# Performance work log

Hardware: AMD Instinct MI355X
Metric: run time of the kernel (lower is better)

The kernel has to match this reference:

```python
import jax, jax.numpy as jnp
import numpy as np

N = 100000   # nodes
E = 800000   # edges
IN = 256     # input feature dim
H = 4        # heads per layer
D = 32       # per-head hidden dim (num_hidden)
SLOPE = 0.2  # leaky_relu negative slope


def setup_inputs() -> dict:
    key = jax.random.key(0)
    ks = jax.random.split(key, 8)
    s = 0.1  # weight scale for numerical stability
    x = jax.random.normal(ks[0], (N, IN), jnp.float32)
    edge_index = jax.random.randint(ks[1], (2, E), 0, N, dtype=jnp.int32)
    W0 = jax.random.normal(ks[2], (IN, H * D), jnp.float32) * s
    al0 = jax.random.normal(ks[3], (H, D), jnp.float32) * s
    ar0 = jax.random.normal(ks[4], (H, D), jnp.float32) * s
    W1 = jax.random.normal(ks[5], (H * D, H * D), jnp.float32) * s
    al1 = jax.random.normal(ks[6], (H, D), jnp.float32) * s
    ar1 = jax.random.normal(ks[7], (H, D), jnp.float32) * s
    return {"x": x, "edge_index": edge_index, "W0": W0, "al0": al0,
            "ar0": ar0, "W1": W1, "al1": al1, "ar1": ar1}


def _gat_layer(h, W, al, ar, src, dst, residual):
    """One GATConv: project, edge attention, dst-wise softmax, scatter-agg."""
    n = h.shape[0]
    feat = (h @ W).reshape(n, H, D)              # [N,H,D]
    el = jnp.einsum('nhd,hd->nh', feat, al)      # [N,H]
    er = jnp.einsum('nhd,hd->nh', feat, ar)      # [N,H]
    e = jax.nn.leaky_relu(el[src] + er[dst], SLOPE)   # raw scores [E,H]
    # edge softmax grouped by destination node (numerically stable)
    emax = jax.ops.segment_max(e, dst, num_segments=n)   # [N,H]
    eexp = jnp.exp(e - emax[dst])                          # [E,H]
    denom = jax.ops.segment_sum(eexp, dst, num_segments=n)  # [N,H]
    a = eexp / denom[dst]                                  # attention [E,H]
    msg = feat[src] * a[:, :, None]                        # [E,H,D]
    rst = jax.ops.segment_sum(msg, dst, num_segments=n)    # [N,H,D]
    if residual:
        rst = rst + h.reshape(n, H, D)  # identity residual (dims match)
    rst = jax.nn.elu(rst)               # activation
    return rst, a, e


def reference(x, edge_index, W0, al0, ar0, W1, al1, ar1):
    src, dst = edge_index[0], edge_index[1]
    # layer 0: no residual
    h1, a0, e0 = _gat_layer(x, W0, al0, ar0, src, dst, residual=False)
    atten0 = e0.mean(axis=-1)  # e_gat.flatten(1).mean(-1) -> [E]
    # layer 1: residual
    h2, a1, e1 = _gat_layer(h1.reshape(N, H * D), W1, al1, ar1, src, dst,
                            residual=True)
    atten1 = e1.mean(axis=-1)
    temp = h2.reshape(N, H * D)          # flattened node embeddings
    heads = tuple(h2[:, i] for i in range(H))  # per-head [N,D]
    return (temp,) + heads + (e1, atten0, atten1)
```

## Files before the change

kernel.cpp:

```cpp
#include <hip/hip_runtime.h>
#include <hip/hip_bf16.h>


typedef _Float16 f16;
typedef _Float16 f16x2 __attribute__((ext_vector_type(2)));
typedef _Float16 f16x8 __attribute__((ext_vector_type(8)));
typedef float f32x2 __attribute__((ext_vector_type(2)));
typedef float f32x4 __attribute__((ext_vector_type(4)));

__device__ __forceinline__ void gload16(const void* g, void* l) {
    __builtin_amdgcn_global_load_lds(
        (const __attribute__((address_space(1))) unsigned int*)g,
        (__attribute__((address_space(3))) unsigned int*)l, 16, 0, 0);
}

__global__ void prep(const float* __restrict__ W0, const float* __restrict__ W1,
                     f16* __restrict__ Wth0, f16* __restrict__ Wtl0,
                     f16* __restrict__ Wth1, f16* __restrict__ Wtl1,
                     const int* __restrict__ dsts, int* __restrict__ deg, int E) {
    int i = blockIdx.x * blockDim.x + threadIdx.x;
    if (i < 256 * 128) {
        int k = i >> 7, c = i & 127;
        float v = W0[i];
        f16 h = (f16)v;
        Wth0[(size_t)c * 256 + k] = h;
        Wtl0[(size_t)c * 256 + k] = (f16)(v - (float)h);
    } else if (i < 256 * 128 + 128 * 128) {
        int j = i - 256 * 128;
        int k = j >> 7, c = j & 127;
        float v = W1[j];
        f16 h = (f16)v;
        Wth1[(size_t)c * 128 + k] = h;
        Wtl1[(size_t)c * 128 + k] = (f16)(v - (float)h);
    } else {
        int e = i - (256 * 128 + 128 * 128);
        if (e < E) atomicAdd(&deg[dsts[e]], 1);
    }
}

template <int AFP16>
__global__ __launch_bounds__(256, 2) void gemm_mfma(
        const void* __restrict__ Xv, const f16* __restrict__ Wth,
        const f16* __restrict__ Wtl, f16* __restrict__ Y16,
        const float* __restrict__ al, const float* __restrict__ ar,
        float* __restrict__ el_out, float* __restrict__ er_out,
        int nrows, int K) {
    __shared__ float As32[AFP16 ? 1 : 128 * 32];
    __shared__ f16   As16[AFP16 ? 128 * 32 : 1];
    __shared__ f16   Bh[128 * 32];
    __shared__ f16   Bl[128 * 32];
    const int t    = threadIdx.x;
    const int wave = t >> 6;
    const int lane = t & 63;
    const int lr   = lane & 15;
    const int kg   = lane >> 4;
    const int row0 = blockIdx.x * 128;

    f32x4 acc[2][8];
    #pragma unroll
    for (int i = 0; i < 2; ++i)
        #pragma unroll
        for (int j = 0; j < 8; ++j) acc[i][j] = (f32x4){0.f, 0.f, 0.f, 0.f};

    for (int k0 = 0; k0 < K; k0 += 32) {
        if constexpr (!AFP16) {
            #pragma unroll
            for (int j = 0; j < 4; ++j) {
                int G = t + 256 * j;
                int row = G >> 3, slot = G & 7;
                int g = slot ^ (row & 7);
                int grow = row0 + row; if (grow >= nrows) grow = nrows - 1;
                gload16((const float*)Xv + (size_t)grow * K + k0 + g * 4,
                        &As32[G * 4]);
            }
        } else {
            #pragma unroll
            for (int j = 0; j < 2; ++j) {
                int G = t + 256 * j;
                int row = G >> 2, g4 = G & 3;
                int grow = row0 + row; if (grow >= nrows) grow = nrows - 1;
                gload16((const f16*)Xv + (size_t)grow * K + k0 + g4 * 8,
                        &As16[G * 8]);
            }
        }
        #pragma unroll
        for (int j = 0; j < 2; ++j) {
            int G = t + 256 * j;
            int r = G >> 2, g4 = G & 3;
            int p = ((r & 15) << 3) | (r >> 4);
            gload16(Wth + (size_t)p * K + k0 + g4 * 8, &Bh[G * 8]);
            gload16(Wtl + (size_t)p * K + k0 + g4 * 8, &Bl[G * 8]);
        }
        __syncthreads();

        const int ar0_ = wave * 32 + lr;
        f16x8 ah0, ah1, alo0, alo1;
        if constexpr (!AFP16) {
            int s0 = (2 * kg) ^ (lr & 7);
            int s1 = (2 * kg + 1) ^ (lr & 7);
            f32x4 u0 = *(const f32x4*)&As32[ar0_ * 32 + s0 * 4];
            f32x4 u1 = *(const f32x4*)&As32[ar0_ * 32 + s1 * 4];
            f32x4 v0 = *(const f32x4*)&As32[(ar0_ + 16) * 32 + s0 * 4];
            f32x4 v1 = *(const f32x4*)&As32[(ar0_ + 16) * 32 + s1 * 4];
            float a8[8] = {u0[0], u0[1], u0[2], u0[3], u1[0], u1[1], u1[2], u1[3]};
            float b8[8] = {v0[0], v0[1], v0[2], v0[3], v1[0], v1[1], v1[2], v1[3]};
            #pragma unroll
            for (int i = 0; i < 8; ++i) {
                f16 h0 = (f16)a8[i]; ah0[i] = h0; alo0[i] = (f16)(a8[i] - (float)h0);
                f16 h1 = (f16)b8[i]; ah1[i] = h1; alo1[i] = (f16)(b8[i] - (float)h1);
            }
        } else {
            ah0 = *(const f16x8*)&As16[ar0_ * 32 + kg * 8];
            ah1 = *(const f16x8*)&As16[(ar0_ + 16) * 32 + kg * 8];
        }
        f16x8 bh[8];
        #pragma unroll
        for (int cb = 0; cb < 8; ++cb)
            bh[cb] = *(const f16x8*)&Bh[(cb * 16 + lr) * 32 + kg * 8];

        #pragma unroll
        for (int cb = 0; cb < 8; ++cb) {
            acc[0][cb] = __builtin_amdgcn_mfma_f32_16x16x32_f16(ah0, bh[cb], acc[0][cb], 0, 0, 0);
            acc[1][cb] = __builtin_amdgcn_mfma_f32_16x16x32_f16(ah1, bh[cb], acc[1][cb], 0, 0, 0);
        }
        if constexpr (!AFP16) {
            #pragma unroll
            for (int cb = 0; cb < 8; ++cb) {
                acc[0][cb] = __builtin_amdgcn_mfma_f32_16x16x32_f16(alo0, bh[cb], acc[0][cb], 0, 0, 0);
                acc[1][cb] = __builtin_amdgcn_mfma_f32_16x16x32_f16(alo1, bh[cb], acc[1][cb], 0, 0, 0);
            }
        }
        #pragma unroll
        for (int cb = 0; cb < 8; ++cb) {
            f16x8 bl = *(const f16x8*)&Bl[(cb * 16 + lr) * 32 + kg * 8];
            acc[0][cb] = __builtin_amdgcn_mfma_f32_16x16x32_f16(ah0, bl, acc[0][cb], 0, 0, 0);
            acc[1][cb] = __builtin_amdgcn_mfma_f32_16x16x32_f16(ah1, bl, acc[1][cb], 0, 0, 0);
        }
        __syncthreads();
    }

    const int hh = lr >> 2;
    const int co = (lr & 3) * 8;
    float alv[8], arv[8];
    #pragma unroll
    for (int j = 0; j < 8; ++j) {
        alv[j] = al[hh * 32 + co + j];
        arv[j] = ar[hh * 32 + co + j];
    }
    #pragma unroll
    for (int rb = 0; rb < 2; ++rb) {
        int rbase = row0 + wave * 32 + rb * 16 + kg * 4;
        #pragma unroll
        for (int r = 0; r < 4; ++r) {
            int grow = rbase + r;
            f16x8 hv;
            float sl_ = 0.0f, sr_ = 0.0f;
            #pragma unroll
            for (int cb = 0; cb < 8; ++cb) {
                float v = acc[rb][cb][r];
                hv[cb] = (f16)v;
                sl_ += v * alv[cb];
                sr_ += v * arv[cb];
            }
            sl_ += __shfl_xor(sl_, 1); sl_ += __shfl_xor(sl_, 2);
            sr_ += __shfl_xor(sr_, 1); sr_ += __shfl_xor(sr_, 2);
            if (grow < nrows) {
                *(f16x8*)(Y16 + (size_t)grow * 128 + lr * 8) = hv;
                if ((lane & 3) == 0) {
                    el_out[4 * (size_t)grow + hh] = sl_;
                    er_out[4 * (size_t)grow + hh] = sr_;
                }
            }
        }
    }
}

__global__ __launch_bounds__(256) void scan_block(const int* __restrict__ deg,
                                                  int* __restrict__ excl,
                                                  int* __restrict__ bsums, int n) {
    __shared__ int wsums[4];
    int t = threadIdx.x;
    int base = blockIdx.x * 1024;
    int idx = base + t * 4;
    int v[4];
    #pragma unroll
    for (int i = 0; i < 4; ++i) v[i] = (idx + i < n) ? deg[idx + i] : 0;
    int tsum = v[0] + v[1] + v[2] + v[3];
    int lane = t & 63, wid = t >> 6;
    int incl = tsum;
    #pragma unroll
    for (int off = 1; off < 64; off <<= 1) {
        int u = __shfl_up(incl, off, 64);
        if (lane >= off) incl += u;
    }
    if (lane == 63) wsums[wid] = incl;
    __syncthreads();
    if (t == 0) {
        int s = 0;
        #pragma unroll
        for (int w = 0; w < 4; ++w) { int x = wsums[w]; wsums[w] = s; s += x; }
    }
    __syncthreads();
    int ex = incl - tsum + wsums[wid];
    int run = ex;
    #pragma unroll
    for (int i = 0; i < 4; ++i) { if (idx + i < n) excl[idx + i] = run; run += v[i]; }
    if (t == 255) bsums[blockIdx.x] = ex + tsum;
}

__global__ __launch_bounds__(256) void scan_fin(int* __restrict__ row_off,
                                                const int* __restrict__ bsums,
                                                int* __restrict__ cursor,
                                                int n, int nb) {
    __shared__ int spfx;
    int b = blockIdx.x;
    int t = threadIdx.x;
    if (t < 64) {
        int v = 0;
        if (t < b && t < nb) v = bsums[t];
        int t2 = t + 64;
        if (t2 < b && t2 < nb) v += bsums[t2];
        #pragma unroll
        for (int off = 32; off; off >>= 1) v += __shfl_xor(v, off, 64);
        if (t == 0) spfx = v;
    }
    __syncthreads();
    int pfx = spfx;
    int base = b * 1024 + t * 4;
    #pragma unroll
    for (int i2 = 0; i2 < 4; ++i2) {
        int i = base + i2;
        if (i < n) {
            int v = row_off[i] + pfx;
            row_off[i] = v;
            cursor[i]  = v;
        }
    }
}

__global__ void fill_csr_edge0(const int* __restrict__ srcs, const int* __restrict__ dsts,
                               int* __restrict__ cursor, int* __restrict__ csr_src,
                               const float* __restrict__ el, const float* __restrict__ er,
                               float* __restrict__ atten0, int E) {
    int e = blockIdx.x * blockDim.x + threadIdx.x;
    if (e >= E) return;
    int s = srcs[e], d = dsts[e];
    int p = atomicAdd(&cursor[d], 1);
    csr_src[p] = s;
    float4 elv = *(const float4*)(el + 4 * (size_t)s);
    float4 erv = *(const float4*)(er + 4 * (size_t)d);
    float v0 = elv.x + erv.x, v1 = elv.y + erv.y;
    float v2 = elv.z + erv.z, v3 = elv.w + erv.w;
    v0 = v0 > 0.0f ? v0 : 0.2f * v0;
    v1 = v1 > 0.0f ? v1 : 0.2f * v1;
    v2 = v2 > 0.0f ? v2 : 0.2f * v2;
    v3 = v3 > 0.0f ? v3 : 0.2f * v3;
    __builtin_nontemporal_store((v0 + v1 + v2 + v3) * 0.25f, atten0 + e);
}

__global__ void edge1_kernel(const int* __restrict__ srcs, const int* __restrict__ dsts,
                             const float* __restrict__ el, const float* __restrict__ er,
                             float* __restrict__ e1_out, float* __restrict__ atten1,
                             int E) {
    int e = blockIdx.x * blockDim.x + threadIdx.x;
    if (e >= E) return;
    int s = srcs[e], d = dsts[e];
    float4 elv = *(const float4*)(el + 4 * (size_t)s);
    float4 erv = *(const float4*)(er + 4 * (size_t)d);
    float v0 = elv.x + erv.x, v1 = elv.y + erv.y;
    float v2 = elv.z + erv.z, v3 = elv.w + erv.w;
    v0 = v0 > 0.0f ? v0 : 0.2f * v0;
    v1 = v1 > 0.0f ? v1 : 0.2f * v1;
    v2 = v2 > 0.0f ? v2 : 0.2f * v2;
    v3 = v3 > 0.0f ? v3 : 0.2f * v3;
    __builtin_nontemporal_store((f32x4){v0, v1, v2, v3},
                                (f32x4*)(e1_out + 4 * (size_t)e));
    __builtin_nontemporal_store((v0 + v1 + v2 + v3) * 0.25f, atten1 + e);
}

template <int LAYER>
__global__ __launch_bounds__(256) void aggregate(const int* __restrict__ row_off,
                                                 const int* __restrict__ deg,
                                                 const int* __restrict__ csr_src,
                                                 const float* __restrict__ el,
                                                 const float* __restrict__ er,
                                                 const f16* __restrict__ feat16,
                                                 const f16* __restrict__ resid16,
                                                 f16* __restrict__ out16,
                                                 float* __restrict__ out32,
                                                 float* __restrict__ heads,
                                                 int N) {
    int wave = (blockIdx.x * 256 + threadIdx.x) >> 6;
    if (wave >= N) return;
    int lane = threadIdx.x & 63;
    int q  = lane >> 4;
    int sc = lane & 15;
    int h  = sc >> 2;
    int start = row_off[wave];
    int dc    = deg[wave];
    float er_h = er[4 * (size_t)wave + h];

    float acc[8];
    #pragma unroll
    for (int j = 0; j < 8; ++j) acc[j] = 0.0f;
    float dh = 0.0f;

    for (int cs = 0; cs < dc; cs += 64) {
        int act = dc - cs; if (act > 64) act = 64;
        int sl = (lane < act) ? csr_src[start + cs + lane] : 0;
        int i = 0;
        for (; i + 8 <= act; i += 8) {
            int s0 = __shfl(sl, i + q);
            int s1 = __shfl(sl, i + 4 + q);
            float x0 = el[4 * (size_t)s0 + h] + er_h;
            float x1 = el[4 * (size_t)s1 + h] + er_h;
            x0 = x0 > 0.0f ? x0 : 0.2f * x0;
            x1 = x1 > 0.0f ? x1 : 0.2f * x1;
            float w0 = __expf(x0);
            float w1 = __expf(x1);
            f16x8 f0 = *(const f16x8*)(feat16 + 128 * (size_t)s0 + sc * 8);
            f16x8 f1 = *(const f16x8*)(feat16 + 128 * (size_t)s1 + sc * 8);
            #pragma unroll
            for (int j = 0; j < 8; ++j) acc[j] += w0 * (float)f0[j];
            #pragma unroll
            for (int j = 0; j < 8; ++j) acc[j] += w1 * (float)f1[j];
            dh += w0 + w1;
        }
        for (; i < act; i += 4) {
            int e = i + q;
            bool on = e < act;
            int s = __shfl(sl, on ? e : 0);
            float x = el[4 * (size_t)s + h] + er_h;
            x = x > 0.0f ? x : 0.2f * x;
            float w = on ? __expf(x) : 0.0f;
            f16x8 fv = *(const f16x8*)(feat16 + 128 * (size_t)s + sc * 8);
            #pragma unroll
            for (int j = 0; j < 8; ++j) acc[j] += w * (float)fv[j];
            dh += w;
        }
    }

    #pragma unroll
    for (int j = 0; j < 8; ++j) {
        acc[j] += __shfl_xor(acc[j], 16);
        acc[j] += __shfl_xor(acc[j], 32);
    }
    dh += __shfl_xor(dh, 16);
    dh += __shfl_xor(dh, 32);

    float inv = (dc > 0) ? 1.0f / dh : 0.0f;
    float ax = (q == 0) ? acc[0] : (q == 1) ? acc[2] : (q == 2) ? acc[4] : acc[6];
    float ay = (q == 0) ? acc[1] : (q == 1) ? acc[3] : (q == 2) ? acc[5] : acc[7];
    ax *= inv; ay *= inv;
    int c0 = sc * 8 + q * 2;
    size_t o = 128 * (size_t)wave + c0;
    if (LAYER == 1) {
        f16x2 rv = *(const f16x2*)(resid16 + o);
        ax += (float)rv[0]; ay += (float)rv[1];
    }
    ax = ax > 0.0f ? ax : __expf(ax) - 1.0f;
    ay = ay > 0.0f ? ay : __expf(ay) - 1.0f;
    if (LAYER == 0) {
        f16x2 hv; hv[0] = (f16)ax; hv[1] = (f16)ay;
        *(f16x2*)(out16 + o) = hv;
    } else {
        __builtin_nontemporal_store((f32x2){ax, ay}, (f32x2*)(out32 + o));
        __builtin_nontemporal_store(
            (f32x2){ax, ay},
            (f32x2*)(heads + (size_t)h * N * 32 + (size_t)wave * 32 + (c0 & 31)));
    }
}

extern "C" void kernel_launch(void* const* d_in, const int* in_sizes, int n_in,
                              void* d_out, int out_size, void* d_ws, size_t ws_size,
                              hipStream_t stream) {
    const float* x   = (const float*)d_in[0];
    const int*   ei  = (const int*)d_in[1];
    const float* W0  = (const float*)d_in[2];
    const float* al0 = (const float*)d_in[3];
    const float* ar0 = (const float*)d_in[4];
    const float* W1  = (const float*)d_in[5];
    const float* al1 = (const float*)d_in[6];
    const float* ar1 = (const float*)d_in[7];

    const int N = in_sizes[0] / 256;
    const int E = in_sizes[1] / 2;
    const size_t NF = (size_t)N * 128;

    const int* srcs = ei;
    const int* dsts = ei + E;

    float* out = (float*)d_out;
    f16*   f16ws  = (f16*)d_ws;
    f16*   feat16 = f16ws;
    f16*   h1_16  = feat16 + NF;
    float* el   = (float*)(h1_16 + NF);
    float* er   = el + (size_t)N * 4;
    f16*   wth0 = (f16*)(er + (size_t)N * 4);
    f16*   wtl0 = wth0 + (size_t)128 * 256;
    f16*   wth1 = wtl0 + (size_t)128 * 256;
    f16*   wtl1 = wth1 + (size_t)128 * 128;
    int*   ints    = (int*)(wtl1 + (size_t)128 * 128);
    int*   deg     = ints;
    int*   row_off = deg + N;
    int*   cursor  = row_off + N;
    int*   csr_src = cursor + N;
    int*   bsums   = csr_src + E;

    float* heads      = out + NF;
    float* e1_out     = out + 2 * NF;
    float* atten0_out = e1_out + (size_t)E * 4;
    float* atten1_out = atten0_out + E;

    hipMemsetAsync(deg, 0, (size_t)N * sizeof(int), stream);
    const int wtot = 256 * 128 + 128 * 128;
    prep<<<(wtot + E + 255) / 256, 256, 0, stream>>>(W0, W1, wth0, wtl0, wth1, wtl1,
                                                     dsts, deg, E);
    int nb = (N + 1023) / 1024;
    scan_block<<<nb, 256, 0, stream>>>(deg, row_off, bsums, N);
    scan_fin<<<nb, 256, 0, stream>>>(row_off, bsums, cursor, N, nb);

    const int gemm_blocks = (N + 127) / 128;
    const int agg_blocks  = (N + 3) / 4;

    gemm_mfma<0><<<gemm_blocks, 256, 0, stream>>>(x, wth0, wtl0, feat16, al0, ar0,
                                                  el, er, N, 256);
    fill_csr_edge0<<<(E + 255) / 256, 256, 0, stream>>>(srcs, dsts, cursor, csr_src,
                                                        el, er, atten0_out, E);
    aggregate<0><<<agg_blocks, 256, 0, stream>>>(row_off, deg, csr_src, el, er,
                                                 feat16, nullptr, h1_16, nullptr,
                                                 nullptr, N);

    gemm_mfma<1><<<gemm_blocks, 256, 0, stream>>>(h1_16, wth1, wtl1, feat16, al1, ar1,
                                                  el, er, N, 128);
    edge1_kernel<<<(E + 255) / 256, 256, 0, stream>>>(srcs, dsts, el, er,
                                                      e1_out, atten1_out, E);
    aggregate<1><<<agg_blocks, 256, 0, stream>>>(row_off, deg, csr_src, el, er,
                                                 feat16, h1_16, nullptr, out,
                                                 heads, N);
}
```

Baseline: 427.0 us.

## Co-launch scan with layer-0 GEMM and edge1 with layer-1 aggregation

Merges the block scan into the layer-0 GEMM launch and the layer-1 edge-score kernel into the layer-1 aggregation launch, selecting the role by block index. The aggregation now computes degree from row_off[n+1]-row_off[n], so a sentinel entry is written at the end of row_off. The goal is fewer launches and letting small independent kernels overlap with large ones. The scan blocks share the GEMM's launch bounds and LDS footprint, and every aggregate block now does an extra row_off load.

```diff
diff --git a/kernel.cpp b/kernel.cpp
--- a/kernel.cpp
+++ b/kernel.cpp
@@ -39,8 +39,8 @@
 }
 
 template <int AFP16>
-__global__ __launch_bounds__(256, 2) void gemm_mfma(
-        const void* __restrict__ Xv, const f16* __restrict__ Wth,
+__device__ __forceinline__ void gemm_body(
+        int bid, const void* __restrict__ Xv, const f16* __restrict__ Wth,
         const f16* __restrict__ Wtl, f16* __restrict__ Y16,
         const float* __restrict__ al, const float* __restrict__ ar,
         float* __restrict__ el_out, float* __restrict__ er_out,
@@ -54,7 +54,7 @@
     const int lane = t & 63;
     const int lr   = lane & 15;
     const int kg   = lane >> 4;
-    const int row0 = blockIdx.x * 128;
+    const int row0 = bid * 128;
 
     f32x4 acc[2][8];
     #pragma unroll
@@ -175,12 +175,12 @@
     }
 }
 
-__global__ __launch_bounds__(256) void scan_block(const int* __restrict__ deg,
-                                                  int* __restrict__ excl,
-                                                  int* __restrict__ bsums, int n) {
+__device__ __forceinline__ void scan_body(int b, const int* __restrict__ deg,
+                                          int* __restrict__ excl,
+                                          int* __restrict__ bsums, int n) {
     __shared__ int wsums[4];
     int t = threadIdx.x;
-    int base = blockIdx.x * 1024;
+    int base = b * 1024;
     int idx = base + t * 4;
     int v[4];
     #pragma unroll
@@ -205,12 +205,36 @@
     int run = ex;
     #pragma unroll
     for (int i = 0; i < 4; ++i) { if (idx + i < n) excl[idx + i] = run; run += v[i]; }
-    if (t == 255) bsums[blockIdx.x] = ex + tsum;
+    if (t == 255) bsums[b] = ex + tsum;
+}
+
+__global__ __launch_bounds__(256, 2) void gemm0_scan(
+        const float* __restrict__ X, const f16* __restrict__ Wth,
+        const f16* __restrict__ Wtl, f16* __restrict__ Y16,
+        const float* __restrict__ al, const float* __restrict__ ar,
+        float* __restrict__ el_out, float* __restrict__ er_out,
+        int nrows, int K, int gblocks,
+        const int* __restrict__ deg, int* __restrict__ excl,
+        int* __restrict__ bsums, int n) {
+    if ((int)blockIdx.x < gblocks)
+        gemm_body<0>(blockIdx.x, X, Wth, Wtl, Y16, al, ar, el_out, er_out, nrows, K);
+    else
+        scan_body(blockIdx.x - gblocks, deg, excl, bsums, n);
+}
+
+__global__ __launch_bounds__(256, 2) void gemm_mfma1(
+        const f16* __restrict__ X, const f16* __restrict__ Wth,
+        const f16* __restrict__ Wtl, f16* __restrict__ Y16,
+        const float* __restrict__ al, const float* __restrict__ ar,
+        float* __restrict__ el_out, float* __restrict__ er_out,
+        int nrows, int K) {
+    gemm_body<1>(blockIdx.x, X, Wth, Wtl, Y16, al, ar, el_out, er_out, nrows, K);
 }
 
 __global__ __launch_bounds__(256) void scan_fin(int* __restrict__ row_off,
                                                 const int* __restrict__ bsums,
                                                 int* __restrict__ cursor,
+                                                const int* __restrict__ deg,
                                                 int n, int nb) {
     __shared__ int spfx;
     int b = blockIdx.x;
@@ -234,6 +258,7 @@
             int v = row_off[i] + pfx;
             row_off[i] = v;
             cursor[i]  = v;
+            if (i == n - 1) row_off[n] = v + deg[i];
         }
     }
 }
@@ -258,11 +283,11 @@
     __builtin_nontemporal_store((v0 + v1 + v2 + v3) * 0.25f, atten0 + e);
 }
 
-__global__ void edge1_kernel(const int* __restrict__ srcs, const int* __restrict__ dsts,
-                             const float* __restrict__ el, const float* __restrict__ er,
-                             float* __restrict__ e1_out, float* __restrict__ atten1,
-                             int E) {
-    int e = blockIdx.x * blockDim.x + threadIdx.x;
+__device__ __forceinline__ void edge1_body(int bid,
+        const int* __restrict__ srcs, const int* __restrict__ dsts,
+        const float* __restrict__ el, const float* __restrict__ er,
+        float* __restrict__ e1_out, float* __restrict__ atten1, int E) {
+    int e = bid * 256 + threadIdx.x;
     if (e >= E) return;
     int s = srcs[e], d = dsts[e];
     float4 elv = *(const float4*)(el + 4 * (size_t)s);
@@ -279,25 +304,20 @@
 }
 
 template <int LAYER>
-__global__ __launch_bounds__(256) void aggregate(const int* __restrict__ row_off,
-                                                 const int* __restrict__ deg,
-                                                 const int* __restrict__ csr_src,
-                                                 const float* __restrict__ el,
-                                                 const float* __restrict__ er,
-                                                 const f16* __restrict__ feat16,
-                                                 const f16* __restrict__ resid16,
-                                                 f16* __restrict__ out16,
-                                                 float* __restrict__ out32,
-                                                 float* __restrict__ heads,
-                                                 int N) {
-    int wave = (blockIdx.x * 256 + threadIdx.x) >> 6;
+__device__ __forceinline__ void agg_body(int bid,
+        const int* __restrict__ row_off, const int* __restrict__ csr_src,
+        const float* __restrict__ el, const float* __restrict__ er,
+        const f16* __restrict__ feat16, const f16* __restrict__ resid16,
+        f16* __restrict__ out16, float* __restrict__ out32,
+        float* __restrict__ heads, int N) {
+    int wave = (bid * 256 + (int)threadIdx.x) >> 6;
     if (wave >= N) return;
     int lane = threadIdx.x & 63;
     int q  = lane >> 4;
     int sc = lane & 15;
     int h  = sc >> 2;
     int start = row_off[wave];
-    int dc    = deg[wave];
+    int dc    = row_off[wave + 1] - start;
     float er_h = er[4 * (size_t)wave + h];
 
     float acc[8];
@@ -371,6 +391,31 @@
     }
 }
 
+__global__ __launch_bounds__(256) void aggregate0(const int* __restrict__ row_off,
+                                                  const int* __restrict__ csr_src,
+                                                  const float* __restrict__ el,
+                                                  const float* __restrict__ er,
+                                                  const f16* __restrict__ feat16,
+                                                  f16* __restrict__ out16, int N) {
+    agg_body<0>(blockIdx.x, row_off, csr_src, el, er, feat16, nullptr,
+                out16, nullptr, nullptr, N);
+}
+
+__global__ __launch_bounds__(256) void layer1_fused(
+        const int* __restrict__ row_off, const int* __restrict__ csr_src,
+        const float* __restrict__ el, const float* __restrict__ er,
+        const f16* __restrict__ feat16, const f16* __restrict__ resid16,
+        float* __restrict__ out32, float* __restrict__ heads,
+        const int* __restrict__ srcs, const int* __restrict__ dsts,
+        float* __restrict__ e1_out, float* __restrict__ atten1,
+        int aggBlocks, int N, int E) {
+    if ((int)blockIdx.x < aggBlocks)
+        agg_body<1>(blockIdx.x, row_off, csr_src, el, er, feat16, resid16,
+                    nullptr, out32, heads, N);
+    else
+        edge1_body(blockIdx.x - aggBlocks, srcs, dsts, el, er, e1_out, atten1, E);
+}
+
 extern "C" void kernel_launch(void* const* d_in, const int* in_sizes, int n_in,
                               void* d_out, int out_size, void* d_ws, size_t ws_size,
                               hipStream_t stream) {
@@ -403,7 +448,7 @@
     int*   ints    = (int*)(wtl1 + (size_t)128 * 128);
     int*   deg     = ints;
     int*   row_off = deg + N;
-    int*   cursor  = row_off + N;
+    int*   cursor  = row_off + N + 1;
     int*   csr_src = cursor + N;
     int*   bsums   = csr_src + E;
 
@@ -416,26 +461,24 @@
     const int wtot = 256 * 128 + 128 * 128;
     prep<<<(wtot + E + 255) / 256, 256, 0, stream>>>(W0, W1, wth0, wtl0, wth1, wtl1,
                                                      dsts, deg, E);
-    int nb = (N + 1023) / 1024;
-    scan_block<<<nb, 256, 0, stream>>>(deg, row_off, bsums, N);
-    scan_fin<<<nb, 256, 0, stream>>>(row_off, bsums, cursor, N, nb);
 
     const int gemm_blocks = (N + 127) / 128;
     const int agg_blocks  = (N + 3) / 4;
-
-    gemm_mfma<0><<<gemm_blocks, 256, 0, stream>>>(x, wth0, wtl0, feat16, al0, ar0,
-                                                  el, er, N, 256);
-    fill_csr_edge0<<<(E + 255) / 256, 256, 0, stream>>>(srcs, dsts, cursor, csr_src,
-                                                        el, er, atten0_out, E);
-    aggregate<0><<<agg_blocks, 256, 0, stream>>>(row_off, deg, csr_src, el, er,
-                                                 feat16, nullptr, h1_16, nullptr,
-                                                 nullptr, N);
-
-    gemm_mfma<1><<<gemm_blocks, 256, 0, stream>>>(h1_16, wth1, wtl1, feat16, al1, ar1,
-                                                  el, er, N, 128);
-    edge1_kernel<<<(E + 255) / 256, 256, 0, stream>>>(srcs, dsts, el, er,
-                                                      e1_out, atten1_out, E);
-    aggregate<1><<<agg_blocks, 256, 0, stream>>>(row_off, deg, csr_src, el, er,
-                                                 feat16, h1_16, nullptr, out,
-                                                 heads, N);
-}
+    const int edge_blocks = (E + 255) / 256;
+    const int nb = (N + 1023) / 1024;
+
+    gemm0_scan<<<gemm_blocks + nb, 256, 0, stream>>>(x, wth0, wtl0, feat16, al0, ar0,
+                                                     el, er, N, 256, gemm_blocks,
+                                                     deg, row_off, bsums, N);
+    scan_fin<<<nb, 256, 0, stream>>>(row_off, bsums, cursor, deg, N, nb);
+    fill_csr_edge0<<<edge_blocks, 256, 0, stream>>>(srcs, dsts, cursor, csr_src,
+                                                    el, er, atten0_out, E);
+    aggregate0<<<agg_blocks, 256, 0, stream>>>(row_off, csr_src, el, er,
+                                               feat16, h1_16, N);
+
+    gemm_mfma1<<<gemm_blocks, 256, 0, stream>>>(h1_16, wth1, wtl1, feat16, al1, ar1,
+                                                el, er, N, 128);
+    layer1_fused<<<agg_blocks + edge_blocks, 256, 0, stream>>>(
+        row_off, csr_src, el, er, feat16, h1_16, out, heads,
+        srcs, dsts, e1_out, atten1_out, agg_blocks, N, E);
+}
```

Result: faster. 416.2 us (-2.5%).
